# Kernel optimization log

Hardware: AMD Instinct MI355X
Metric: run time of the kernel (lower is better)

Reference implementation:

```python
import jax, jax.numpy as jnp
import numpy as np

# dims: layers, batch, seq_len, num_nodes, n_experts, top_k, expert hidden, pred_len
LAYERS, B, L, N, E, K, DFF, P = 3, 32, 336, 321, 4, 2, 512, 96
LOSS_COEF = 0.01
INV_SQRT2 = 0.7071067811865476


def setup_inputs() -> dict:
    key = jax.random.key(0)
    ks = jax.random.split(key, 10)
    w = lambda k, shape: (jax.random.normal(k, shape, jnp.float32) * 0.02)
    return {
        "x": jax.random.normal(ks[0], (B, L, N, 1), jnp.float32),
        "noise": jax.random.normal(ks[1], (LAYERS, B, E), jnp.float32),
        "w_gate": w(ks[2], (LAYERS, L, E)),
        "w_noise": w(ks[3], (LAYERS, L, E)),
        "W1": w(ks[4], (LAYERS, E, L, DFF)),
        "b1": jnp.zeros((LAYERS, E, DFF), jnp.float32),
        "W2": w(ks[5], (LAYERS, E, DFF, L)),
        "b2": jnp.zeros((LAYERS, E, L), jnp.float32),
        "p1w": w(ks[6], (P, L)),
        "p1b": jnp.zeros((P,), jnp.float32),
        "p2w": w(ks[7], (2 * P, P)),
        "p2b": jnp.zeros((2 * P,), jnp.float32),
    }


def _cv_sq(v):
    # squared coefficient of variation (unbiased var, matches torch .var())
    return jnp.var(v, ddof=1) / (jnp.mean(v) ** 2 + 1e-10)


def _norm_cdf(z):
    return 0.5 * (1.0 + jax.lax.erf(z * jnp.asarray(INV_SQRT2, z.dtype)))


def _ams_layer(x, noise, wg, wn, W1, b1, W2, b2):
    # x: [B, L, N] -> [B, L, N]; noisy top-k gated MoE over the time axis
    g = x.mean(axis=2)                                   # [B, L] gate features
    clean = g @ wg                                       # [B, E]
    nstd = jax.nn.softplus(g @ wn) + 1e-2                # [B, E]
    noisy = clean + noise * nstd                         # [B, E]

    top_logits, top_idx = jax.lax.top_k(noisy, K + 1)    # [B, K+1]
    gates_k = jax.nn.softmax(top_logits[:, :K], axis=-1)
    gates = jnp.zeros_like(noisy).at[
        jnp.arange(noisy.shape[0])[:, None], top_idx[:, :K]
    ].set(gates_k)                                       # dense [B, E], zeros off top-k

    importance = gates.sum(axis=0)
    thr_in = top_logits[:, K][:, None]                   # (k+1)-th value
    thr_out = top_logits[:, K - 1][:, None]              # k-th value
    is_in = noisy > thr_in
    load = jnp.where(
        is_in,
        _norm_cdf((clean - thr_in) / nstd),
        _norm_cdf((clean - thr_out) / nstd),
    ).sum(axis=0)
    aux = LOSS_COEF * (_cv_sq(importance) + _cv_sq(load))

    # experts: per-node MLP along time dim, evaluated densely and combined by gates
    xT = x.transpose(0, 2, 1)                            # [B, N, L]
    h = jax.nn.gelu(jnp.einsum('bnl,eld->ebnd', xT, W1) + b1[:, None, None, :])
    y = jnp.einsum('ebnd,edl->ebnl', h, W2) + b2[:, None, None, :]
    out = jnp.einsum('be,ebnl->bln', gates, y) + x       # residual connection
    return out, aux


def reference(x, noise, w_gate, w_noise, W1, b1, W2, b2, p1w, p1b, p2w, p2b):
    x0 = x[..., 0]                                       # [B, L, N]
    # RevIN norm (affine=False): per-sample, per-node stats over time
    mu = x0.mean(axis=1, keepdims=True)
    sd = jnp.sqrt(x0.var(axis=1, keepdims=True) + 1e-5)
    out = (x0 - mu) / sd

    balance_loss = jnp.asarray(0.0, jnp.float32)
    for l in range(LAYERS):
        out, aux = _ams_layer(out, noise[l], w_gate[l], w_noise[l],
                              W1[l], b1[l], W2[l], b2[l])
        balance_loss = balance_loss + aux

    # projection head: [B, N, L] -> [B, N, 2P] -> [B, P, N, 2]
    h = jnp.tanh(out.transpose(0, 2, 1) @ p1w.T + p1b)
    proj = (h @ p2w.T + p2b).reshape(out.shape[0], N, P, 2).transpose(0, 2, 1, 3)
    mean_out = proj[..., 0]
    std_out = jax.nn.softplus(proj[..., 1]) + 1e-6
    return mean_out, balance_loss, std_out
```

## Files before the change

kernel.cpp:

```cpp
#include <hip/hip_runtime.h>
#include <hip/hip_bf16.h>

#define NLAYERS 3
#define BB 32
#define LL 336
#define LP 352
#define NN 321
#define EE 4
#define DHID 512
#define PP 96
#define STOT (BB*NN*LL)
#define MROWS (BB*NN)
#define BPN ((size_t)BB*PP*NN)

#define F1S 5632
#define E1S 180224
#define F2S 8192
#define E2S 172032

typedef __attribute__((ext_vector_type(8))) short short8;
typedef __attribute__((ext_vector_type(4))) float float4v;

union BF { __hip_bfloat16 h; short s; };

__device__ __forceinline__ short f2b(float f) { BF u; u.h = __float2bfloat16(f); return u.s; }

__device__ __forceinline__ float fast_tanh(float y) {
    float e = __expf(2.0f * y);
    return 1.0f - 2.0f / (e + 1.0f);
}
__device__ __forceinline__ float gelu_f(float x) {
    return 0.5f * x * (1.0f + fast_tanh(0.7978845608028654f * (x + 0.044715f * x * x * x)));
}
__device__ __forceinline__ float softplus_f(float x) {
    return fmaxf(x, 0.0f) + log1pf(expf(-fabsf(x)));
}

__global__ __launch_bounds__(256) void prep_kernel(
    const float* __restrict__ x, const float* __restrict__ W1, const float* __restrict__ W2,
    const float* __restrict__ p1w, const float* __restrict__ p2w,
    float* __restrict__ MU, float* __restrict__ IV, float* __restrict__ LOSS,
    float* __restrict__ G0, short* __restrict__ W1f, short* __restrict__ W2f,
    short* __restrict__ p1wb, short* __restrict__ p2wb)
{
    __shared__ short Ws[64][72];
    __shared__ float Ss[4][64], Sq[4][64];
    int idx = blockIdx.x, tid = threadIdx.x;
    if (idx < 1152) {
        const float* src; int K, D, KS, bx, by, le;
        if (idx < 576) {
            le = idx / 48; int r = idx % 48;
            src = W1 + (size_t)le * LL * DHID;
            K = LL; D = DHID; KS = LP; bx = r % 8; by = r / 8;
        } else {
            int s2 = idx - 576; le = s2 / 48; int r = s2 % 48;
            src = W2 + (size_t)le * DHID * LL;
            K = DHID; D = LL; KS = DHID; bx = r % 6; by = r / 6;
        }
        int d0 = bx * 64, k0 = by * 64;
        #pragma unroll
        for (int i = 0; i < 16; ++i) {
            int lin = tid + i * 256;
            int ki = lin >> 6, dj = lin & 63;
            int k = k0 + ki, d = d0 + dj;
            Ws[ki][dj] = (k < K && d < D) ? f2b(src[(size_t)k * D + d]) : (short)0;
        }
        __syncthreads();
        int di = tid >> 2, d = d0 + di;
        if (d >= D) return;
        #pragma unroll
        for (int kp = 0; kp < 2; ++kp) {
            int kj = ((tid & 3) + 4 * kp) * 8;
            int k = k0 + kj;
            if (k >= KS) continue;
            union { short s[8]; uint4 u; } pk;
            #pragma unroll
            for (int j = 0; j < 8; ++j) pk.s[j] = Ws[kj + j][di];
            int nf = d >> 4;
            int ks = k >> 5;
            int l  = (((k >> 3) & 3) << 4) | (d & 15);
            if (idx < 576) {
                size_t o = (size_t)le * E1S + ((size_t)(nf * 11 + ks) * 64 + l) * 8;
                *(uint4*)&W1f[o] = pk.u;
            } else {
                size_t o = (size_t)le * E2S + ((size_t)(nf * 16 + ks) * 64 + l) * 8;
                *(uint4*)&W2f[o] = pk.u;
            }
        }
    } else if (idx < 1344) {
        int q = idx - 1152;
        int b = q / 6, nt = q % 6;
        if (tid < 56) G0[q * 56 + tid] = 0.0f;
        if (q == 0 && tid < 8) LOSS[tid] = 0.0f;
        int ni = tid & 63, lc = tid >> 6;
        int n = nt * 64 + ni;
        float s = 0.f, ss = 0.f;
        if (n < NN) {
            const float* xp = x + ((size_t)b * LL + lc * 84) * NN + n;
            for (int l = 0; l < 84; ++l, xp += NN) {
                float v = *xp; s += v; ss = fmaf(v, v, ss);
            }
        }
        Ss[lc][ni] = s; Sq[lc][ni] = ss;
        __syncthreads();
        if (lc == 0 && n < NN) {
            float st = ((Ss[0][ni] + Ss[1][ni]) + Ss[2][ni]) + Ss[3][ni];
            float sq = ((Sq[0][ni] + Sq[1][ni]) + Sq[2][ni]) + Sq[3][ni];
            float mu  = st * (1.0f / LL);
            float var = sq * (1.0f / LL) - mu * mu;
            MU[b * NN + n] = mu;
            IV[b * NN + n] = 1.0f / sqrtf(var + 1e-5f);
        }
    } else {
        int i = (idx - 1344) * 256 + tid;
        if (i < PP * LP) {
            int n = i / LP, k = i - n * LP;
            p1wb[i] = (k < LL) ? f2b(p1w[n * LL + k]) : (short)0;
        } else if (i < PP * LP + 2 * PP * PP) {
            int j = i - PP * LP;
            p2wb[j] = f2b(p2w[j]);
        }
    }
}

__global__ __launch_bounds__(256) void revin_tn(
    const float* __restrict__ x, const float* __restrict__ MU, const float* __restrict__ IV,
    float* __restrict__ T, short* __restrict__ Tb16, float* __restrict__ G0)
{
    int b = blockIdx.x, nt = blockIdx.y, lt = blockIdx.z;
    int n0 = nt * 64, l0 = lt * 48;
    __shared__ float Ls[48][65];
    __shared__ float Vs[48][65];
    int tid = threadIdx.x;
    #pragma unroll
    for (int i = 0; i < 12; ++i) {
        int lin = tid + i * 256;
        int li = lin >> 6, ni = lin & 63;
        int n = n0 + ni;
        Ls[li][ni] = (n < NN) ? x[((size_t)b * LL + l0 + li) * NN + n] : 0.f;
    }
    __syncthreads();
    int r = tid >> 2, q = tid & 3;
    int n = n0 + r;
    bool valid = (n < NN);
    float mu = 0.f, iv = 0.f;
    if (valid) { mu = MU[b * NN + n]; iv = IV[b * NN + n]; }
    size_t rowf = (size_t)(b * NN + (valid ? n : 0)) * LL + l0;
    size_t rowb = (size_t)(b * NN + (valid ? n : 0)) * LP + l0;
    #pragma unroll
    for (int k = 0; k < 3; ++k) {
        int c = (q + 4 * k) * 4;
        float4 v;
        v.x = (Ls[c    ][r] - mu) * iv;
        v.y = (Ls[c + 1][r] - mu) * iv;
        v.z = (Ls[c + 2][r] - mu) * iv;
        v.w = (Ls[c + 3][r] - mu) * iv;
        Vs[c][r] = v.x; Vs[c + 1][r] = v.y; Vs[c + 2][r] = v.z; Vs[c + 3][r] = v.w;
        if (valid) {
            *(float4*)&T[rowf + c] = v;
            union { short s[4]; uint2 u; } pk;
            pk.s[0] = f2b(v.x); pk.s[1] = f2b(v.y); pk.s[2] = f2b(v.z); pk.s[3] = f2b(v.w);
            *(uint2*)&Tb16[rowb + c] = pk.u;
        }
    }
    if (valid && lt == 6 && q == 3) {
        size_t base = (size_t)(b * NN + n) * LP;
        *(uint4*)&Tb16[base + 336] = make_uint4(0, 0, 0, 0);
        *(uint4*)&Tb16[base + 344] = make_uint4(0, 0, 0, 0);
    }
    __syncthreads();
    if (tid < 48) {
        float s = 0.f;
        #pragma unroll 8
        for (int rr = 0; rr < 64; ++rr) s += Vs[tid][rr];
        unsafeAtomicAdd(&G0[b * LL + l0 + tid], s);
    }
}

struct LossSM {
    float pc2[BB][EE][2], pn2[BB][EE][2];
    float sc[BB][EE], sn[BB][EE], sy[BB][EE], sg[BB][EE];
    float sti[BB], sto[BB];
    float simp[EE], sload[EE];
};

__device__ void loss_tail(LossSM* S, const float* __restrict__ Gcur,
                          const float* __restrict__ wgL, const float* __restrict__ wnL,
                          const float* __restrict__ noiseL, float* __restrict__ LOSS, int tid)
{
    __syncthreads();
    {
        int bb = tid >> 3, ee = (tid >> 1) & 3, sub = tid & 1;
        float c = 0.f, nr = 0.f;
        const float* gp = Gcur + bb * LL;
        for (int l = sub * 168; l < sub * 168 + 168; ++l) {
            float gv = gp[l] * (1.0f / NN);
            c  = fmaf(gv, wgL[l * EE + ee], c);
            nr = fmaf(gv, wnL[l * EE + ee], nr);
        }
        S->pc2[bb][ee][sub] = c; S->pn2[bb][ee][sub] = nr;
    }
    __syncthreads();
    if (tid < 128) {
        int bb = tid >> 2, ee = tid & 3;
        float c  = S->pc2[bb][ee][0] + S->pc2[bb][ee][1];
        float nr = S->pn2[bb][ee][0] + S->pn2[bb][ee][1];
        float ns = softplus_f(nr) + 1e-2f;
        S->sc[bb][ee] = c; S->sn[bb][ee] = ns;
        S->sy[bb][ee] = fmaf(noiseL[bb * EE + ee], ns, c);
    }
    __syncthreads();
    if (tid < 128 && (tid & 3) == 0) {
        int bb = tid >> 2;
        float v[4];
        #pragma unroll
        for (int i = 0; i < 4; ++i) v[i] = S->sy[bb][i];
        int i0 = 0;
        for (int i = 1; i < 4; ++i) if (v[i] > v[i0]) i0 = i;
        int i1 = -1;
        for (int i = 0; i < 4; ++i) { if (i == i0) continue; if (i1 < 0 || v[i] > v[i1]) i1 = i; }
        float m3 = -1e30f;
        for (int i = 0; i < 4; ++i) { if (i == i0 || i == i1) continue; if (v[i] > m3) m3 = v[i]; }
        float e1 = expf(v[i1] - v[i0]);
        float invd = 1.0f / (1.0f + e1);
        #pragma unroll
        for (int i = 0; i < 4; ++i) S->sg[bb][i] = 0.f;
        S->sg[bb][i0] = invd;
        S->sg[bb][i1] = e1 * invd;
        S->sti[bb] = m3;
        S->sto[bb] = v[i1];
    }
    __syncthreads();
    if (tid < EE) {
        int ee = tid;
        float imp = 0.f, ld = 0.f;
        for (int bb2 = 0; bb2 < BB; ++bb2) {
            imp += S->sg[bb2][ee];
            float thr = (S->sy[bb2][ee] > S->sti[bb2]) ? S->sti[bb2] : S->sto[bb2];
            float z = (S->sc[bb2][ee] - thr) / S->sn[bb2][ee];
            ld += 0.5f * (1.0f + erff(z * 0.7071067811865476f));
        }
        S->simp[ee] = imp; S->sload[ee] = ld;
    }
    __syncthreads();
    if (tid == 0) {
        float aux = 0.f;
        {
            float m = (S->simp[0] + S->simp[1] + S->simp[2] + S->simp[3]) * 0.25f;
            float var = 0.f;
            for (int i = 0; i < 4; ++i) { float d = S->simp[i] - m; var += d * d; }
            var *= (1.0f / 3.0f);
            aux += var / (m * m + 1e-10f);
        }
        {
            float m = (S->sload[0] + S->sload[1] + S->sload[2] + S->sload[3]) * 0.25f;
            float var = 0.f;
            for (int i = 0; i < 4; ++i) { float d = S->sload[i] - m; var += d * d; }
            var *= (1.0f / 3.0f);
            aux += var / (m * m + 1e-10f);
        }
        LOSS[0] += 0.01f * aux;
    }
}

__global__ __launch_bounds__(256, 4) void fc1_mfma(
    const short* __restrict__ Tb16, const short* __restrict__ W1f_l,
    const float* __restrict__ b1_l,
    const float* __restrict__ Gcur, float* __restrict__ Gnext,
    const float* __restrict__ wgL, const float* __restrict__ wnL,
    const float* __restrict__ noiseL,
    int* __restrict__ IDX, float* __restrict__ GV,
    short* __restrict__ Hs, float* __restrict__ LOSS)
{
    int i = blockIdx.x;
    int low = i & 7, rest = i >> 3;
    int v = rest & 3, ghi = rest >> 2;
    int g = ghi * 8 + low;
    int y = g % 11, b = g / 11;
    int xt = v & 1, slot = v >> 1;
    int m0 = y * 32, n0 = xt * 256;
    int tid = threadIdx.x;
    int wave = tid >> 6, lane = tid & 63, quad = lane >> 4, l16 = lane & 15;
    __shared__ __align__(16) short Al[32][360];
    __shared__ float redc[4][4], redn[4][4];
    if (i < 42) Gnext[i * 256 + tid] = 0.0f;
    {
        #pragma unroll
        for (int it = 0; it < 6; ++it) {
            int idx = tid + it * 256;
            if (idx < 1408) {
                int r = idx / 44, c = (idx - r * 44) * 8;
                int gr = m0 + r; if (gr > NN - 1) gr = NN - 1;
                *(uint4*)&Al[r][c] = *(const uint4*)(Tb16 + ((size_t)b * NN + gr) * LP + c);
            }
        }
    }
    {
        float pce[4] = {0.f,0.f,0.f,0.f}, pne[4] = {0.f,0.f,0.f,0.f};
        const float* gp = Gcur + b * LL;
        #pragma unroll
        for (int pass = 0; pass < 2; ++pass) {
            int l = tid + pass * 256;
            if (l < LL) {
                float gv = gp[l] * (1.0f / NN);
                #pragma unroll
                for (int e2 = 0; e2 < 4; ++e2) {
                    pce[e2] = fmaf(gv, wgL[l * EE + e2], pce[e2]);
                    pne[e2] = fmaf(gv, wnL[l * EE + e2], pne[e2]);
                }
            }
        }
        #pragma unroll
        for (int off = 32; off >= 1; off >>= 1) {
            #pragma unroll
            for (int e2 = 0; e2 < 4; ++e2) {
                pce[e2] += __shfl_xor(pce[e2], off);
                pne[e2] += __shfl_xor(pne[e2], off);
            }
        }
        if (lane == 0) {
            #pragma unroll
            for (int e2 = 0; e2 < 4; ++e2) { redc[wave][e2] = pce[e2]; redn[wave][e2] = pne[e2]; }
        }
    }
    __syncthreads();
    int e; float gt;
    {
        float vv[4];
        #pragma unroll
        for (int e2 = 0; e2 < 4; ++e2) {
            float c  = ((redc[0][e2] + redc[1][e2]) + redc[2][e2]) + redc[3][e2];
            float nr = ((redn[0][e2] + redn[1][e2]) + redn[2][e2]) + redn[3][e2];
            float ns = softplus_f(nr) + 1e-2f;
            vv[e2] = fmaf(noiseL[b * EE + e2], ns, c);
        }
        int i0 = 0;
        #pragma unroll
        for (int e2 = 1; e2 < 4; ++e2) if (vv[e2] > vv[i0]) i0 = e2;
        int i1 = -1;
        #pragma unroll
        for (int e2 = 0; e2 < 4; ++e2) { if (e2 == i0) continue; if (i1 < 0 || vv[e2] > vv[i1]) i1 = e2; }
        float e1v = expf(vv[i1] - vv[i0]);
        float invd = 1.0f / (1.0f + e1v);
        e  = slot ? i1 : i0;
        gt = slot ? (e1v * invd) : invd;
        if (y == 0 && v == 0 && tid == 0) {
            IDX[2 * b] = i0; IDX[2 * b + 1] = i1;
            GV[2 * b] = invd; GV[2 * b + 1] = e1v * invd;
        }
    }

    const short* Bf = W1f_l + (size_t)(e * 32 + xt * 16 + wave * 4) * F1S + lane * 8;
    float4v zero4 = {0.f, 0.f, 0.f, 0.f};
    float4v acc[2][4];
    #pragma unroll
    for (int a = 0; a < 2; ++a)
        #pragma unroll
        for (int j = 0; j < 4; ++j) acc[a][j] = zero4;

    short8 bc[4];
    #pragma unroll
    for (int j = 0; j < 4; ++j) bc[j] = *(const short8*)(Bf + j * F1S);
    #pragma unroll
    for (int ks = 0; ks < 11; ++ks) {
        short8 bn[4];
        if (ks < 10) {
            int o = (ks + 1) * 512;
            #pragma unroll
            for (int j = 0; j < 4; ++j) bn[j] = *(const short8*)(Bf + j * F1S + o);
        }
        int off = ks * 32;
        short8 af[2];
        #pragma unroll
        for (int mi = 0; mi < 2; ++mi) af[mi] = *(const short8*)&Al[mi * 16 + l16][off + quad * 8];
        #pragma unroll
        for (int mi = 0; mi < 2; ++mi) {
            acc[mi][0] = __builtin_amdgcn_mfma_f32_16x16x32_bf16(af[mi], bc[0], acc[mi][0], 0, 0, 0);
            acc[mi][1] = __builtin_amdgcn_mfma_f32_16x16x32_bf16(af[mi], bc[1], acc[mi][1], 0, 0, 0);
            acc[mi][2] = __builtin_amdgcn_mfma_f32_16x16x32_bf16(af[mi], bc[2], acc[mi][2], 0, 0, 0);
            acc[mi][3] = __builtin_amdgcn_mfma_f32_16x16x32_bf16(af[mi], bc[3], acc[mi][3], 0, 0, 0);
        }
        if (ks < 10) {
            #pragma unroll
            for (int j = 0; j < 4; ++j) bc[j] = bn[j];
        }
    }
    const float* bb = b1_l + (size_t)e * DHID;
    int wn4 = wave * 64;
    float bias[4];
    #pragma unroll
    for (int ni = 0; ni < 4; ++ni) bias[ni] = bb[n0 + wn4 + ni * 16 + l16];
    short* Ho = Hs + (size_t)(b * 2 + slot) * NN * DHID;
    #pragma unroll
    for (int mi = 0; mi < 2; ++mi) {
        #pragma unroll
        for (int r = 0; r < 4; ++r) {
            int gm = m0 + mi * 16 + quad * 4 + r;
            if (gm >= NN) continue;
            #pragma unroll
            for (int ni = 0; ni < 4; ++ni) {
                int gd = n0 + wn4 + ni * 16 + l16;
                float vv = acc[mi][ni][r] + bias[ni];
                Ho[(size_t)gm * DHID + gd] = f2b(gt * gelu_f(vv));
            }
        }
    }
    if (i == 0) loss_tail((LossSM*)&Al[0][0], Gcur, wgL, wnL, noiseL, LOSS, tid);
}

__global__ __launch_bounds__(256, 4) void fc2_fused(
    const short* __restrict__ Hs, const short* __restrict__ W2f_l,
    const float* __restrict__ b2_l, float* __restrict__ T,
    short* __restrict__ Tb16, float* __restrict__ Gnext,
    const int* __restrict__ IDX, const float* __restrict__ GV, int lastL)
{
    int i = blockIdx.x;
    int low = i & 7, rest = i >> 3;
    int v = rest % 3, ghi = rest / 3;
    int g = ghi * 8 + low;
    int y = g % 11, b = g / 11;
    int m0 = y * 32, n0 = v * 128;
    int tid = threadIdx.x;
    int wave = tid >> 6, lane = tid & 63, quad = lane >> 4, l16 = lane & 15;
    int wn = wave * 32;
    __shared__ short Al[32][264];
    int e0 = IDX[2 * b], e1 = IDX[2 * b + 1];
    float gt0 = GV[2 * b], gt1 = GV[2 * b + 1];
    float4v zero4 = {0.f, 0.f, 0.f, 0.f};
    float4v acc[2][2];
    #pragma unroll
    for (int a = 0; a < 2; ++a)
        #pragma unroll
        for (int j = 0; j < 2; ++j) acc[a][j] = zero4;

    int nfr = v * 8 + wave * 2;
    int nf0 = (nfr > 20) ? 20 : nfr;
    int nf1 = (nfr + 1 > 20) ? 20 : nfr + 1;

    int r8 = tid >> 5, c0s = (tid & 31) * 8;
    #pragma unroll
    for (int sc2 = 0; sc2 < 4; ++sc2) {
        int slot = sc2 >> 1, chunk = sc2 & 1;
        int koff = chunk * 256;
        int ez = slot ? e1 : e0;
        const short* As = Hs + ((size_t)(b * 2 + slot) * NN) * DHID + koff;
        #pragma unroll
        for (int a = 0; a < 4; ++a) {
            int rr = a * 8 + r8;
            int gr = m0 + rr; if (gr > NN - 1) gr = NN - 1;
            *(uint4*)&Al[rr][c0s] = *(const uint4*)(As + (size_t)gr * DHID + c0s);
        }
        __syncthreads();
        const short* B0 = W2f_l + (size_t)ez * E2S + (size_t)nf0 * F2S + (size_t)chunk * 4096 + lane * 8;
        const short* B1 = W2f_l + (size_t)ez * E2S + (size_t)nf1 * F2S + (size_t)chunk * 4096 + lane * 8;
        short8 c0 = *(const short8*)(B0);
        short8 c1 = *(const short8*)(B1);
        #pragma unroll
        for (int ks = 0; ks < 8; ++ks) {
            short8 n0v, n1v;
            if (ks < 7) {
                n0v = *(const short8*)(B0 + (ks + 1) * 512);
                n1v = *(const short8*)(B1 + (ks + 1) * 512);
            }
            int off = ks * 32;
            short8 af[2];
            #pragma unroll
            for (int mi = 0; mi < 2; ++mi) af[mi] = *(const short8*)&Al[mi * 16 + l16][off + quad * 8];
            #pragma unroll
            for (int mi = 0; mi < 2; ++mi) {
                acc[mi][0] = __builtin_amdgcn_mfma_f32_16x16x32_bf16(af[mi], c0, acc[mi][0], 0, 0, 0);
                acc[mi][1] = __builtin_amdgcn_mfma_f32_16x16x32_bf16(af[mi], c1, acc[mi][1], 0, 0, 0);
            }
            if (ks < 7) { c0 = n0v; c1 = n1v; }
        }
        __syncthreads();
    }
    const float* b2e0 = b2_l + (size_t)e0 * LL;
    const float* b2e1 = b2_l + (size_t)e1 * LL;
    float* Tb = T + (size_t)b * NN * LL;
    short* Bt = Tb16 + (size_t)b * NN * LP;
    #pragma unroll
    for (int ni = 0; ni < 2; ++ni) {
        int gl = n0 + wn + ni * 16 + l16;
        float s = 0.f;
        if (gl < LL) {
            float bias = gt0 * b2e0[gl] + gt1 * b2e1[gl];
            #pragma unroll
            for (int mi = 0; mi < 2; ++mi) {
                #pragma unroll
                for (int r = 0; r < 4; ++r) {
                    int gm = m0 + mi * 16 + quad * 4 + r;
                    if (gm < NN) {
                        float vv = acc[mi][ni][r] + bias + Tb[(size_t)gm * LL + gl];
                        if (!lastL) Tb[(size_t)gm * LL + gl] = vv;
                        Bt[(size_t)gm * LP + gl] = f2b(vv);
                        s += vv;
                    }
                }
            }
        }
        s += __shfl_xor(s, 16);
        s += __shfl_xor(s, 32);
        if (!lastL && quad == 0 && gl < LL)
            unsafeAtomicAdd(&Gnext[b * LL + gl], s);
    }
}

__global__ __launch_bounds__(256) void proj_fused(
    const short* __restrict__ Tb16,
    const short* __restrict__ p1wb, const float* __restrict__ p1b,
    const short* __restrict__ p2wb, const float* __restrict__ p2b,
    float* __restrict__ out, const float* __restrict__ LOSS)
{
    __shared__ short Al[32][360];
    __shared__ short Hp[32][104];
    int m0 = blockIdx.x * 32;
    int tid = threadIdx.x;
    if (blockIdx.x == 0 && tid == 0) out[BPN] = LOSS[0];
    int wave = tid >> 6, lane = tid & 63, quad = lane >> 4, l16 = lane & 15;
    float4v zero4 = {0.f, 0.f, 0.f, 0.f};

    #pragma unroll
    for (int i = 0; i < 6; ++i) {
        int idx = tid + i * 256;
        if (idx < 1408) {
            int r = idx / 44, c = (idx - r * 44) * 8;
            *(uint4*)&Al[r][c] = *(const uint4*)(Tb16 + (size_t)(m0 + r) * LP + c);
        }
    }
    __syncthreads();

    {
        int rf = wave & 1, cfb = wave >> 1;
        float4v acc1[3];
        #pragma unroll
        for (int j = 0; j < 3; ++j) acc1[j] = zero4;
        const short* B1p0 = p1wb + (size_t)(cfb * 16 + l16) * LP + quad * 8;
        #pragma unroll
        for (int ks = 0; ks < 11; ++ks) {
            int off = ks * 32;
            short8 af = *(const short8*)&Al[rf * 16 + l16][off + quad * 8];
            #pragma unroll
            for (int j = 0; j < 3; ++j) {
                short8 bf = *(const short8*)(B1p0 + (size_t)j * 32 * LP + off);
                acc1[j] = __builtin_amdgcn_mfma_f32_16x16x32_bf16(af, bf, acc1[j], 0, 0, 0);
            }
        }
        #pragma unroll
        for (int j = 0; j < 3; ++j) {
            int p = (cfb + 2 * j) * 16 + l16;
            float pb = p1b[p];
            #pragma unroll
            for (int r = 0; r < 4; ++r)
                Hp[rf * 16 + quad * 4 + r][p] = f2b(fast_tanh(acc1[j][r] + pb));
        }
    }
    __syncthreads();

    float4v acc2[3][2];
    #pragma unroll
    for (int a = 0; a < 3; ++a)
        #pragma unroll
        for (int j = 0; j < 2; ++j) acc2[a][j] = zero4;
    #pragma unroll
    for (int kc = 0; kc < 3; ++kc) {
        int off = kc * 32 + quad * 8;
        short8 bfv0 = *(const short8*)&Hp[l16][off];
        short8 bfv1 = *(const short8*)&Hp[16 + l16][off];
        #pragma unroll
        for (int mi = 0; mi < 3; ++mi) {
            int cf = wave * 3 + mi;
            short8 af = *(const short8*)(p2wb + (size_t)(cf * 16 + l16) * PP + off);
            acc2[mi][0] = __builtin_amdgcn_mfma_f32_16x16x32_bf16(af, bfv0, acc2[mi][0], 0, 0, 0);
            acc2[mi][1] = __builtin_amdgcn_mfma_f32_16x16x32_bf16(af, bfv1, acc2[mi][1], 0, 0, 0);
        }
    }
    int bqv[2], ndv[2];
    #pragma unroll
    for (int ni = 0; ni < 2; ++ni) {
        int gm = m0 + ni * 16 + l16;
        int bq = gm / NN;
        bqv[ni] = bq; ndv[ni] = gm - bq * NN;
    }
    #pragma unroll
    for (int mi = 0; mi < 3; ++mi) {
        #pragma unroll
        for (int r = 0; r < 4; ++r) {
            int c = (wave * 3 + mi) * 16 + quad * 4 + r;
            float pb = p2b[c];
            int p = c >> 1;
            if ((r & 1) == 0) {
                #pragma unroll
                for (int ni = 0; ni < 2; ++ni) {
                    float v = acc2[mi][ni][r] + pb;
                    out[((size_t)bqv[ni] * PP + p) * NN + ndv[ni]] = v;
                }
            } else {
                #pragma unroll
                for (int ni = 0; ni < 2; ++ni) {
                    float v = acc2[mi][ni][r] + pb;
                    out[BPN + 1 + ((size_t)bqv[ni] * PP + p) * NN + ndv[ni]] = softplus_f(v) + 1e-6f;
                }
            }
        }
    }
}

extern "C" void kernel_launch(void* const* d_in, const int* in_sizes, int n_in,
                              void* d_out, int out_size, void* d_ws, size_t ws_size,
                              hipStream_t stream)
{
    const float* x     = (const float*)d_in[0];
    const float* noise = (const float*)d_in[1];
    const float* wg    = (const float*)d_in[2];
    const float* wn    = (const float*)d_in[3];
    const float* W1    = (const float*)d_in[4];
    const float* b1    = (const float*)d_in[5];
    const float* W2    = (const float*)d_in[6];
    const float* b2    = (const float*)d_in[7];
    const float* p1w   = (const float*)d_in[8];
    const float* p1b   = (const float*)d_in[9];
    const float* p2w   = (const float*)d_in[10];
    const float* p2b   = (const float*)d_in[11];
    float* out = (float*)d_out;

    float* ws   = (float*)d_ws;
    float* T    = ws;
    float* G0   = T + STOT;
    float* G1   = G0 + BB * LL;
    float* LOSS = G1 + BB * LL;
    float* GV   = LOSS + 8;
    int*   IDX  = (int*)(GV + 64);
    float* MU   = (float*)(IDX + 64);
    float* IV   = MU + MROWS;
    short* W1f  = (short*)(IV + MROWS);
    short* W2f  = W1f + (size_t)NLAYERS * EE * DHID * LP;
    short* p1wb = W2f + (size_t)NLAYERS * EE * LL * DHID;
    short* p2wb = p1wb + PP * LP;
    short* Tb16 = p2wb + 2 * PP * PP;
    short* Hs   = Tb16 + (size_t)(MROWS + 64) * LP;

    prep_kernel<<<1549, 256, 0, stream>>>(x, W1, W2, p1w, p2w, MU, IV, LOSS, G0,
                                          W1f, W2f, p1wb, p2wb);
    revin_tn<<<dim3(BB, 6, 7), 256, 0, stream>>>(x, MU, IV, T, Tb16, G0);

    for (int l = 0; l < NLAYERS; ++l) {
        const float* Gcur = (l == 1) ? G1 : G0;
        float* Gnext      = (l == 1) ? G0 : G1;
        fc1_mfma<<<1408, 256, 0, stream>>>(
            Tb16, W1f + (size_t)l * EE * E1S, b1 + (size_t)l * EE * DHID,
            Gcur, Gnext, wg + (size_t)l * LL * EE, wn + (size_t)l * LL * EE,
            noise + (size_t)l * BB * EE, IDX, GV, Hs, LOSS);
        fc2_fused<<<1056, 256, 0, stream>>>(
            Hs, W2f + (size_t)l * EE * E2S, b2 + (size_t)l * EE * LL,
            T, Tb16, Gnext, IDX, GV, (l == NLAYERS - 1) ? 1 : 0);
    }
    proj_fused<<<321, 256, 0, stream>>>(Tb16, p1wb, p1b, p2wb, p2b, out, LOSS);
}
```

Measured before the change: 297.7 us.

## Process both top-k expert slots per fc1 block and vectorize weight prep loads

Each fc1 block now loops over both selected expert slots, instead of having separate blocks per slot. The grid is halved, and the A-tile staging into shared memory plus the gate logits and top-k computation are done once per tile rather than twice. Separately, the weight prep kernel reads fp32 weights as float4 and writes packed bf16 pairs to shared memory. In exchange, each block does twice the MFMA work serially, and fewer blocks are available to hide latency.

```diff
diff --git a/kernel.cpp b/kernel.cpp
--- a/kernel.cpp
+++ b/kernel.cpp
@@ -59,11 +59,24 @@
         }
         int d0 = bx * 64, k0 = by * 64;
         #pragma unroll
-        for (int i = 0; i < 16; ++i) {
-            int lin = tid + i * 256;
-            int ki = lin >> 6, dj = lin & 63;
+        for (int it = 0; it < 4; ++it) {
+            int ki = (tid >> 4) + it * 16;
+            int dj = (tid & 15) * 4;
             int k = k0 + ki, d = d0 + dj;
-            Ws[ki][dj] = (k < K && d < D) ? f2b(src[(size_t)k * D + d]) : (short)0;
+            float4 v = make_float4(0.f, 0.f, 0.f, 0.f);
+            if (k < K) {
+                const float* sp = src + (size_t)k * D + d;
+                if (d + 3 < D) v = *(const float4*)sp;
+                else {
+                    if (d     < D) v.x = sp[0];
+                    if (d + 1 < D) v.y = sp[1];
+                    if (d + 2 < D) v.z = sp[2];
+                    if (d + 3 < D) v.w = sp[3];
+                }
+            }
+            union { short s[4]; uint2 u; } pk4;
+            pk4.s[0] = f2b(v.x); pk4.s[1] = f2b(v.y); pk4.s[2] = f2b(v.z); pk4.s[3] = f2b(v.w);
+            *(uint2*)&Ws[ki][dj] = pk4.u;
         }
         __syncthreads();
         int di = tid >> 2, d = d0 + di;
@@ -274,10 +287,9 @@
 {
     int i = blockIdx.x;
     int low = i & 7, rest = i >> 3;
-    int v = rest & 3, ghi = rest >> 2;
+    int xt = rest & 1, ghi = rest >> 1;
     int g = ghi * 8 + low;
     int y = g % 11, b = g / 11;
-    int xt = v & 1, slot = v >> 1;
     int m0 = y * 32, n0 = xt * 256;
     int tid = threadIdx.x;
     int wave = tid >> 6, lane = tid & 63, quad = lane >> 4, l16 = lane & 15;
@@ -324,7 +336,7 @@
         }
     }
     __syncthreads();
-    int e; float gt;
+    int i0, i1; float gtv0, gtv1;
     {
         float vv[4];
         #pragma unroll
@@ -334,74 +346,78 @@
             float ns = softplus_f(nr) + 1e-2f;
             vv[e2] = fmaf(noiseL[b * EE + e2], ns, c);
         }
-        int i0 = 0;
+        i0 = 0;
         #pragma unroll
         for (int e2 = 1; e2 < 4; ++e2) if (vv[e2] > vv[i0]) i0 = e2;
-        int i1 = -1;
+        i1 = -1;
         #pragma unroll
         for (int e2 = 0; e2 < 4; ++e2) { if (e2 == i0) continue; if (i1 < 0 || vv[e2] > vv[i1]) i1 = e2; }
         float e1v = expf(vv[i1] - vv[i0]);
         float invd = 1.0f / (1.0f + e1v);
-        e  = slot ? i1 : i0;
-        gt = slot ? (e1v * invd) : invd;
-        if (y == 0 && v == 0 && tid == 0) {
+        gtv0 = invd; gtv1 = e1v * invd;
+        if (y == 0 && xt == 0 && tid == 0) {
             IDX[2 * b] = i0; IDX[2 * b + 1] = i1;
-            GV[2 * b] = invd; GV[2 * b + 1] = e1v * invd;
-        }
-    }
-
-    const short* Bf = W1f_l + (size_t)(e * 32 + xt * 16 + wave * 4) * F1S + lane * 8;
+            GV[2 * b] = gtv0; GV[2 * b + 1] = gtv1;
+        }
+    }
+
+    int wn4 = wave * 64;
     float4v zero4 = {0.f, 0.f, 0.f, 0.f};
-    float4v acc[2][4];
-    #pragma unroll
-    for (int a = 0; a < 2; ++a)
-        #pragma unroll
-        for (int j = 0; j < 4; ++j) acc[a][j] = zero4;
-
-    short8 bc[4];
-    #pragma unroll
-    for (int j = 0; j < 4; ++j) bc[j] = *(const short8*)(Bf + j * F1S);
-    #pragma unroll
-    for (int ks = 0; ks < 11; ++ks) {
-        short8 bn[4];
-        if (ks < 10) {
-            int o = (ks + 1) * 512;
-            #pragma unroll
-            for (int j = 0; j < 4; ++j) bn[j] = *(const short8*)(Bf + j * F1S + o);
-        }
-        int off = ks * 32;
-        short8 af[2];
-        #pragma unroll
-        for (int mi = 0; mi < 2; ++mi) af[mi] = *(const short8*)&Al[mi * 16 + l16][off + quad * 8];
+    #pragma unroll 1
+    for (int slot = 0; slot < 2; ++slot) {
+        int e = slot ? i1 : i0;
+        float gt = slot ? gtv1 : gtv0;
+        const short* Bf = W1f_l + (size_t)(e * 32 + xt * 16 + wave * 4) * F1S + lane * 8;
+        float4v acc[2][4];
+        #pragma unroll
+        for (int a = 0; a < 2; ++a)
+            #pragma unroll
+            for (int j = 0; j < 4; ++j) acc[a][j] = zero4;
+
+        short8 bc[4];
+        #pragma unroll
+        for (int j = 0; j < 4; ++j) bc[j] = *(const short8*)(Bf + j * F1S);
+        #pragma unroll
+        for (int ks = 0; ks < 11; ++ks) {
+            short8 bn[4];
+            if (ks < 10) {
+                int o = (ks + 1) * 512;
+                #pragma unroll
+                for (int j = 0; j < 4; ++j) bn[j] = *(const short8*)(Bf + j * F1S + o);
+            }
+            int off = ks * 32;
+            short8 af[2];
+            #pragma unroll
+            for (int mi = 0; mi < 2; ++mi) af[mi] = *(const short8*)&Al[mi * 16 + l16][off + quad * 8];
+            #pragma unroll
+            for (int mi = 0; mi < 2; ++mi) {
+                acc[mi][0] = __builtin_amdgcn_mfma_f32_16x16x32_bf16(af[mi], bc[0], acc[mi][0], 0, 0, 0);
+                acc[mi][1] = __builtin_amdgcn_mfma_f32_16x16x32_bf16(af[mi], bc[1], acc[mi][1], 0, 0, 0);
+                acc[mi][2] = __builtin_amdgcn_mfma_f32_16x16x32_bf16(af[mi], bc[2], acc[mi][2], 0, 0, 0);
+                acc[mi][3] = __builtin_amdgcn_mfma_f32_16x16x32_bf16(af[mi], bc[3], acc[mi][3], 0, 0, 0);
+            }
+            if (ks < 10) {
+                #pragma unroll
+                for (int j = 0; j < 4; ++j) bc[j] = bn[j];
+            }
+        }
+        const float* bb = b1_l + (size_t)e * DHID;
+        float bias[4];
+        #pragma unroll
+        for (int ni = 0; ni < 4; ++ni) bias[ni] = bb[n0 + wn4 + ni * 16 + l16];
+        short* Ho = Hs + (size_t)(b * 2 + slot) * NN * DHID;
         #pragma unroll
         for (int mi = 0; mi < 2; ++mi) {
-            acc[mi][0] = __builtin_amdgcn_mfma_f32_16x16x32_bf16(af[mi], bc[0], acc[mi][0], 0, 0, 0);
-            acc[mi][1] = __builtin_amdgcn_mfma_f32_16x16x32_bf16(af[mi], bc[1], acc[mi][1], 0, 0, 0);
-            acc[mi][2] = __builtin_amdgcn_mfma_f32_16x16x32_bf16(af[mi], bc[2], acc[mi][2], 0, 0, 0);
-            acc[mi][3] = __builtin_amdgcn_mfma_f32_16x16x32_bf16(af[mi], bc[3], acc[mi][3], 0, 0, 0);
-        }
-        if (ks < 10) {
-            #pragma unroll
-            for (int j = 0; j < 4; ++j) bc[j] = bn[j];
-        }
-    }
-    const float* bb = b1_l + (size_t)e * DHID;
-    int wn4 = wave * 64;
-    float bias[4];
-    #pragma unroll
-    for (int ni = 0; ni < 4; ++ni) bias[ni] = bb[n0 + wn4 + ni * 16 + l16];
-    short* Ho = Hs + (size_t)(b * 2 + slot) * NN * DHID;
-    #pragma unroll
-    for (int mi = 0; mi < 2; ++mi) {
-        #pragma unroll
-        for (int r = 0; r < 4; ++r) {
-            int gm = m0 + mi * 16 + quad * 4 + r;
-            if (gm >= NN) continue;
-            #pragma unroll
-            for (int ni = 0; ni < 4; ++ni) {
-                int gd = n0 + wn4 + ni * 16 + l16;
-                float vv = acc[mi][ni][r] + bias[ni];
-                Ho[(size_t)gm * DHID + gd] = f2b(gt * gelu_f(vv));
+            #pragma unroll
+            for (int r = 0; r < 4; ++r) {
+                int gm = m0 + mi * 16 + quad * 4 + r;
+                if (gm >= NN) continue;
+                #pragma unroll
+                for (int ni = 0; ni < 4; ++ni) {
+                    int gd = n0 + wn4 + ni * 16 + l16;
+                    float vv = acc[mi][ni][r] + bias[ni];
+                    Ho[(size_t)gm * DHID + gd] = f2b(gt * gelu_f(vv));
+                }
             }
         }
     }
@@ -647,7 +663,7 @@
     for (int l = 0; l < NLAYERS; ++l) {
         const float* Gcur = (l == 1) ? G1 : G0;
         float* Gnext      = (l == 1) ? G0 : G1;
-        fc1_mfma<<<1408, 256, 0, stream>>>(
+        fc1_mfma<<<704, 256, 0, stream>>>(
             Tb16, W1f + (size_t)l * EE * E1S, b1 + (size_t)l * EE * DHID,
             Gcur, Gnext, wg + (size_t)l * LL * EE, wn + (size_t)l * LL * EE,
             noise + (size_t)l * BB * EE, IDX, GV, Hs, LOSS);
```

Result: slower. 389.2 us (+30.7%).
